# Optimization experiments

Hardware: AMD Instinct MI355X
Metric: run time of the kernel (lower is better)

## Reference

```python
import jax, jax.numpy as jnp
import numpy as np

N = 20000          # nodes
E = 320000         # edges
IN_C = 512         # input features
HID = 512          # 2*out_channels (first GCN layer width)
OUT = 256          # out_channels == num_hidden
PROJ = 256         # num_proj_hidden


def _gcn_conv(x, W, b, src, dst):
    """PyG GCNConv: x' = D^{-1/2}(A+I)D^{-1/2} X W + b (self-loops added)."""
    n = x.shape[0]
    x = x @ W  # [N, F_out]
    ones = jnp.ones((src.shape[0],), x.dtype)
    deg = jax.ops.segment_sum(ones, dst, num_segments=n) + 1.0  # +1 self-loop
    dis = jax.lax.rsqrt(deg)
    coef = dis[src] * dis[dst]                      # [E]
    agg = jax.ops.segment_sum(x[src] * coef[:, None], dst, num_segments=n)
    agg = agg + x * (dis * dis)[:, None]            # self-loop messages
    return agg + b


def setup_inputs() -> dict:
    key = jax.random.key(0)
    ks = jax.random.split(key, 12)
    s = 0.02
    return {
        "node_features": jax.random.normal(ks[0], (N, IN_C), jnp.float32),
        "edge_index": jax.random.randint(ks[1], (2, E), 0, N, jnp.int64),
        "W1": jax.random.normal(ks[2], (IN_C, HID), jnp.float32) * s,
        "b1": jnp.zeros((HID,), jnp.float32),
        "W2": jax.random.normal(ks[3], (HID, OUT), jnp.float32) * s,
        "b2": jnp.zeros((OUT,), jnp.float32),
        "a": jnp.asarray(0.25, jnp.float32),  # shared PReLU weight
        "W3": jax.random.normal(ks[4], (OUT, PROJ), jnp.float32) * s,
        "b3": jnp.zeros((PROJ,), jnp.float32),
        "W4": jax.random.normal(ks[5], (PROJ, OUT), jnp.float32) * s,
        "b4": jnp.zeros((OUT,), jnp.float32),
    }


def reference(node_features, edge_index, W1, b1, W2, b2, a, W3, b3, W4, b4):
    src, dst = edge_index[0], edge_index[1]
    prelu = lambda x: jnp.where(x > 0, x, a * x)
    h = prelu(_gcn_conv(node_features, W1, b1, src, dst))
    h = prelu(_gcn_conv(h, W2, b2, src, dst))
    # projection MLP: Linear -> ELU -> Linear
    h2 = jax.nn.elu(h @ W3 + b3)
    return h2 @ W4 + b4
```

## Files before the change

kernel.cpp:

```cpp
#include <hip/hip_runtime.h>

typedef unsigned short u16;
typedef unsigned int   u32;
typedef __attribute__((ext_vector_type(8))) short short8;
typedef __attribute__((ext_vector_type(4))) float f32x4;

__device__ __forceinline__ float bf2f(u16 h){
    return __uint_as_float(((u32)h) << 16);
}
__device__ __forceinline__ u16 f2bf(float f){
    u32 u = __float_as_uint(f);
    u += 0x7fffu + ((u >> 16) & 1u);
    return (u16)(u >> 16);
}

__global__ void probe_all(const u16* __restrict__ w1, const int* __restrict__ ei,
                          const void* b1, const void* b2, const void* b3,
                          const void* b4, const void* av,
                          int* __restrict__ f32f, int* __restrict__ efmt,
                          int* __restrict__ zf, int* __restrict__ cnt, int N,
                          u16* d1, u16* d2, u16* d3, u16* d4, u16* da){
    __shared__ int sf32, sfmt;
    int t = threadIdx.x;
    if (t == 0){ sf32 = 0; sfmt = 0; }
    __syncthreads();
    for (int i = t; i < N; i += 256) cnt[i] = 0;
    {
        int huge = 0;
        #pragma unroll
        for (int k = 0; k < 16; k++){
            u16 h = w1[t * 16 + k];
            if (((h >> 7) & 0xFF) >= 0x7F) huge = 1;
        }
        if (huge) atomicOr(&sf32, 1);
    }
    if (ei[2*t + 1] != 0) atomicOr(&sfmt, 1);
    __syncthreads();
    int f32 = sf32, fmt = sfmt;
    if (t == 0){ f32f[0] = f32; efmt[0] = fmt; zf[0] = 0; }
    #define CV(s,i) (f32 ? f2bf(((const float*)(s))[i]) : ((const u16*)(s))[i])
    d1[t]       = CV(b1, t);
    d1[t + 256] = CV(b1, t + 256);
    d2[t] = CV(b2, t);
    d3[t] = CV(b3, t);
    d4[t] = CV(b4, t);
    if (t == 0) da[0] = CV(av, 0);
    #undef CV
}

__device__ __forceinline__ int eload(const int* ei, int fmt, int idx){
    return fmt ? ei[idx] : ei[2*idx];
}

__global__ void deg_count(const int* __restrict__ ei, const int* __restrict__ efmt,
                          int* __restrict__ cnt, int E, int N){
    int e = blockIdx.x * 256 + threadIdx.x;
    if (e < E){
        int d = eload(ei, efmt[0], E + e);
        if ((unsigned)d < (unsigned)N) atomicAdd(&cnt[d], 1);
    }
}

__global__ void scan1(const int* __restrict__ cnt, int* __restrict__ incl,
                      int* __restrict__ bsum, int N){
    __shared__ int s[256];
    int t = threadIdx.x, i = blockIdx.x * 256 + t;
    int v = (i < N) ? cnt[i] : 0;
    s[t] = v;
    __syncthreads();
    #pragma unroll
    for (int off = 1; off < 256; off <<= 1){
        int u = (t >= off) ? s[t - off] : 0;
        __syncthreads();
        s[t] += u;
        __syncthreads();
    }
    if (i < N) incl[i] = s[t];
    if (t == 255) bsum[blockIdx.x] = s[255];
}

__global__ void scan23(const int* __restrict__ cnt, const int* __restrict__ incl,
                       const int* __restrict__ bsum, int nb,
                       int* __restrict__ rowstart, int* __restrict__ cursor,
                       float* __restrict__ dis, int N){
    __shared__ int s[128];
    int t = threadIdx.x;
    if (t < 128) s[t] = (t < nb) ? bsum[t] : 0;
    __syncthreads();
    #pragma unroll
    for (int off = 1; off < 128; off <<= 1){
        int u = 0;
        if (t < 128 && t >= off) u = s[t - off];
        __syncthreads();
        if (t < 128) s[t] += u;
        __syncthreads();
    }
    int boffb = s[blockIdx.x] - bsum[blockIdx.x];
    int i = blockIdx.x * 256 + t;
    if (i < N){
        int v = cnt[i];
        int rsv = boffb + incl[i] - v;
        rowstart[i] = rsv;
        cursor[i]   = rsv;
        dis[i] = rsqrtf((float)v + 1.0f);
    }
    if (blockIdx.x == 0 && t == 0) rowstart[N] = s[nb - 1];
}

__global__ void csr_fill(const int* __restrict__ ei, const int* __restrict__ efmt,
                         int* __restrict__ cursor, int* __restrict__ csr_src,
                         int E, int N){
    int e = blockIdx.x * 256 + threadIdx.x;
    if (e < E){
        int fmt = efmt[0];
        int d = eload(ei, fmt, E + e);
        if ((unsigned)d < (unsigned)N){
            int p = atomicAdd(&cursor[d], 1);
            csr_src[p] = eload(ei, fmt, e);
        }
    }
}

__global__ void transpose_all(const void* w1, const void* w2, const void* w3,
                              const void* w4, const int* __restrict__ flag,
                              u16* o1, u16* o2, u16* o3, u16* o4){
    const void* in; u16* out; int K, N;
    switch (blockIdx.z){
        case 0:  in = w1; out = o1; K = 512; N = 512; break;
        case 1:  in = w2; out = o2; K = 512; N = 256; break;
        case 2:  in = w3; out = o3; K = 256; N = 256; break;
        default: in = w4; out = o4; K = 256; N = 256; break;
    }
    int bx = blockIdx.x * 32;
    int by = blockIdx.y * 32;
    if (bx >= N || by >= K) return;
    __shared__ u16 t[32][33];
    int x = threadIdx.x, y = threadIdx.y;
    int f32 = flag[0];
    #pragma unroll
    for (int i = 0; i < 32; i += 8){
        size_t idx = (size_t)(by + y + i) * N + bx + x;
        t[y + i][x] = f32 ? f2bf(((const float*)in)[idx]) : ((const u16*)in)[idx];
    }
    __syncthreads();
    #pragma unroll
    for (int i = 0; i < 32; i += 8)
        out[(size_t)(bx + y + i) * K + by + x] = t[x][y + i];
}

#define TM 64
#define TN 128
#define BK 32
#define BKP 40

template<int MODE, int OUTF>
__global__ __launch_bounds__(256) void gemm_mfma(
    const void* __restrict__ A, const int* __restrict__ af32,
    const u16* __restrict__ BT,
    const u16* __restrict__ bias, void* __restrict__ Cv,
    int M, int K, int N)
{
    __shared__ __align__(16) u16 As[TM * BKP];
    __shared__ __align__(16) u16 Bs[TN * BKP];
    int tid  = threadIdx.x;
    int lane = tid & 63;
    int wave = tid >> 6;
    int waveM = wave >> 1, waveN = wave & 1;
    int bm = blockIdx.x * TM;
    int bn = blockIdx.y * TN;
    int f32 = af32[0];

    f32x4 acc[2][4] = {};

    int alr = tid >> 2;
    int alc = (tid & 3) * 8;
    int blr = tid >> 1;
    int blc = (tid & 1) * 16;

    for (int k0 = 0; k0 < K; k0 += BK){
        {
            int gr = bm + alr;
            short8 v = {0,0,0,0,0,0,0,0};
            if (gr < M){
                if (f32){
                    const float* p = (const float*)A + (size_t)gr * K + k0 + alc;
                    f32x4 a0 = *(const f32x4*)p;
                    f32x4 a1 = *(const f32x4*)(p + 4);
                    #pragma unroll
                    for (int j = 0; j < 4; j++){
                        v[j]   = (short)f2bf(a0[j]);
                        v[4+j] = (short)f2bf(a1[j]);
                    }
                } else {
                    v = *(const short8*)((const u16*)A + (size_t)gr * K + k0 + alc);
                }
            }
            *(short8*)&As[alr * BKP + alc] = v;
        }
        {
            const u16* p = BT + (size_t)(bn + blr) * K + k0 + blc;
            short8 v0 = *(const short8*)p;
            short8 v1 = *(const short8*)(p + 8);
            *(short8*)&Bs[blr * BKP + blc]     = v0;
            *(short8*)&Bs[blr * BKP + blc + 8] = v1;
        }
        __syncthreads();
        int q = lane >> 4;
        int r16 = lane & 15;
        short8 af[2], bfr[4];
        #pragma unroll
        for (int i = 0; i < 2; i++)
            af[i]  = *(const short8*)&As[(waveM*32 + i*16 + r16) * BKP + q*8];
        #pragma unroll
        for (int j = 0; j < 4; j++)
            bfr[j] = *(const short8*)&Bs[(waveN*64 + j*16 + r16) * BKP + q*8];
        #pragma unroll
        for (int i = 0; i < 2; i++)
            #pragma unroll
            for (int j = 0; j < 4; j++)
                acc[i][j] = __builtin_amdgcn_mfma_f32_16x16x32_bf16(af[i], bfr[j], acc[i][j], 0, 0, 0);
        __syncthreads();
    }

    int q = lane >> 4;
    int c16 = lane & 15;
    #pragma unroll
    for (int i = 0; i < 2; i++){
        #pragma unroll
        for (int j = 0; j < 4; j++){
            int gcol = bn + waveN*64 + j*16 + c16;
            float bvv = (MODE >= 1) ? bf2f(bias[gcol]) : 0.f;
            #pragma unroll
            for (int r = 0; r < 4; r++){
                int grow = bm + waveM*32 + i*16 + q*4 + r;
                if (grow < M){
                    float v = acc[i][j][r] + bvv;
                    if (MODE == 2) v = (v > 0.f) ? v : expm1f(v);
                    if (OUTF) ((float*)Cv)[(size_t)grow * N + gcol] = v;
                    else      ((u16*)Cv)[(size_t)grow * N + gcol] = f2bf(v);
                }
            }
        }
    }
}

template<int F, int NPB>
__global__ __launch_bounds__(F/8*NPB) void aggregate(
    const u16* __restrict__ XW, const int* __restrict__ rowstart,
    const int* __restrict__ csr_src, const float* __restrict__ dis,
    const u16* __restrict__ bias, const u16* __restrict__ aptr,
    u16* __restrict__ out, int N)
{
    int node = blockIdx.x * NPB + threadIdx.y;
    if (node >= N) return;
    int tf = threadIdx.x * 8;
    float a  = bf2f(aptr[0]);
    float di = dis[node];
    int e0 = rowstart[node], e1 = rowstart[node + 1];
    float acc[8] = {0,0,0,0,0,0,0,0};
    int ng = (e1 - e0) >> 3;
    int si[8]; float ci[8];
    if (ng > 0){
        #pragma unroll
        for (int u = 0; u < 8; u++) si[u] = csr_src[e0 + u];
        #pragma unroll
        for (int u = 0; u < 8; u++) ci[u] = dis[si[u]];
    }
    for (int g = 0; g < ng; g++){
        short8 vi[8];
        #pragma unroll
        for (int u = 0; u < 8; u++)
            vi[u] = *(const short8*)(XW + (size_t)si[u] * F + tf);
        int sn[8]; float cn[8];
        bool more = (g + 1) < ng;
        if (more){
            int base = e0 + (g + 1) * 8;
            #pragma unroll
            for (int u = 0; u < 8; u++) sn[u] = csr_src[base + u];
            #pragma unroll
            for (int u = 0; u < 8; u++) cn[u] = dis[sn[u]];
        }
        #pragma unroll
        for (int u = 0; u < 8; u++)
            #pragma unroll
            for (int j = 0; j < 8; j++)
                acc[j] += ci[u] * bf2f((u16)vi[u][j]);
        if (more){
            #pragma unroll
            for (int u = 0; u < 8; u++){ si[u] = sn[u]; ci[u] = cn[u]; }
        }
    }
    int e = e0 + ng * 8;
    for (; e + 4 <= e1; e += 4){
        int s0 = csr_src[e], s1 = csr_src[e+1], s2 = csr_src[e+2], s3 = csr_src[e+3];
        float c0 = dis[s0], c1 = dis[s1], c2 = dis[s2], c3 = dis[s3];
        short8 v0 = *(const short8*)(XW + (size_t)s0 * F + tf);
        short8 v1 = *(const short8*)(XW + (size_t)s1 * F + tf);
        short8 v2 = *(const short8*)(XW + (size_t)s2 * F + tf);
        short8 v3 = *(const short8*)(XW + (size_t)s3 * F + tf);
        #pragma unroll
        for (int j = 0; j < 8; j++)
            acc[j] += c0*bf2f((u16)v0[j]) + c1*bf2f((u16)v1[j])
                    + c2*bf2f((u16)v2[j]) + c3*bf2f((u16)v3[j]);
    }
    for (; e < e1; e++){
        int s = csr_src[e];
        float c = dis[s];
        short8 v = *(const short8*)(XW + (size_t)s * F + tf);
        #pragma unroll
        for (int j = 0; j < 8; j++) acc[j] += c * bf2f((u16)v[j]);
    }
    {
        short8 v = *(const short8*)(XW + (size_t)node * F + tf);
        #pragma unroll
        for (int j = 0; j < 8; j++) acc[j] += di * bf2f((u16)v[j]);
    }
    short8 bv = *(const short8*)(bias + tf);
    short8 o;
    #pragma unroll
    for (int j = 0; j < 8; j++){
        float x = di * acc[j] + bf2f((u16)bv[j]);
        x = (x > 0.f) ? x : a * x;
        o[j] = (short)f2bf(x);
    }
    *(short8*)(out + (size_t)node * F + tf) = o;
}

extern "C" void kernel_launch(void* const* d_in, const int* in_sizes, int n_in,
                              void* d_out, int out_size, void* d_ws, size_t ws_size,
                              hipStream_t stream)
{
    int iX=0, iEI=1, iW1=2, ib1=3, iW2=4, ib2=5, ia=6, iW3=7, ib3=8, iW4=9, ib4=10;
    {
        int jX=-1,jEI=-1,jW1=-1,jb1=-1,jW2=-1,ja=-1,jW3=-1,jW4=-1,jb2=-1,jb3=-1,jb4=-1;
        int n64k=0, n256=0;
        for (int i = 0; i < n_in; i++){
            switch (in_sizes[i]){
                case 10240000: jX = i; break;
                case 640000:   jEI = i; break;
                case 262144:   jW1 = i; break;
                case 131072:   jW2 = i; break;
                case 512:      jb1 = i; break;
                case 1:        ja = i; break;
                case 65536:    if (n64k++ == 0) jW3 = i; else jW4 = i; break;
                case 256: {
                    int k = n256++;
                    if (k == 0) jb2 = i; else if (k == 1) jb3 = i; else jb4 = i;
                } break;
                default: break;
            }
        }
        if (jX>=0&&jEI>=0&&jW1>=0&&jb1>=0&&jW2>=0&&ja>=0&&jW3>=0&&jW4>=0&&jb2>=0&&jb3>=0&&jb4>=0){
            iX=jX; iEI=jEI; iW1=jW1; ib1=jb1; iW2=jW2; ib2=jb2; ia=ja; iW3=jW3; ib3=jb3; iW4=jW4; ib4=jb4;
        }
    }
    int N = in_sizes[iX] / 512;
    int E = in_sizes[iEI] / 2;
    const int* EI = (const int*)d_in[iEI];
    float* OUT = (float*)d_out;
    u16*   S   = (u16*)d_out;

    char* ws = (char*)d_ws;
    size_t off = 0;
    auto alloc = [&](size_t bytes)->char*{
        char* p = ws + off;
        off = (off + bytes + 255) & ~(size_t)255;
        return p;
    };
    int nb = (N + 255) / 256;
    int*   cnt  = (int*)  alloc((size_t)N*4);
    int*   incl = (int*)  alloc((size_t)N*4);
    int*   bsum = (int*)  alloc(512);
    int*   efmt = (int*)  alloc(4);
    int*   f32f = (int*)  alloc(4);
    int*   zf   = (int*)  alloc(4);
    float* dis  = (float*)alloc((size_t)N*4);
    int*   rs   = (int*)  alloc((size_t)(N+1)*4);
    int*   cur  = (int*)  alloc((size_t)N*4);
    int*   csr  = (int*)  alloc((size_t)E*4);
    u16*   WT1  = (u16*)  alloc((size_t)512*512*2);
    u16*   WT2  = (u16*)  alloc((size_t)256*512*2);
    u16*   WT3  = (u16*)  alloc((size_t)256*256*2);
    u16*   WT4  = (u16*)  alloc((size_t)256*256*2);
    u16*   b1c  = (u16*)  alloc((size_t)512*2);
    u16*   b2c  = (u16*)  alloc((size_t)256*2);
    u16*   b3c  = (u16*)  alloc((size_t)256*2);
    u16*   b4c  = (u16*)  alloc((size_t)256*2);
    u16*   ac   = (u16*)  alloc((size_t)8*2);
    u16*   h1   = (u16*)  alloc((size_t)N*512*2);
    u16*   P    = (u16*)  alloc((size_t)N*256*2);

    if (ws_size < off) return;

    probe_all<<<1, 256, 0, stream>>>((const u16*)d_in[iW1], EI,
                                     d_in[ib1], d_in[ib2], d_in[ib3], d_in[ib4],
                                     d_in[ia], f32f, efmt, zf, cnt, N,
                                     b1c, b2c, b3c, b4c, ac);

    int egrid = (E + 255) / 256;
    deg_count<<<egrid, 256, 0, stream>>>(EI, efmt, cnt, E, N);
    scan1<<<nb, 256, 0, stream>>>(cnt, incl, bsum, N);
    scan23<<<nb, 256, 0, stream>>>(cnt, incl, bsum, nb, rs, cur, dis, N);
    csr_fill<<<egrid, 256, 0, stream>>>(EI, efmt, cur, csr, E, N);

    transpose_all<<<dim3(16, 16, 4), dim3(32, 8), 0, stream>>>(
        d_in[iW1], d_in[iW2], d_in[iW3], d_in[iW4], f32f, WT1, WT2, WT3, WT4);

    int gm = (N + TM - 1) / TM;
    dim3 g512(gm, 512 / TN);
    dim3 g256(gm, 256 / TN);

    gemm_mfma<0,0><<<g512, 256, 0, stream>>>(d_in[iX], f32f, WT1, nullptr, S, N, 512, 512);
    aggregate<512,2><<<(N+1)/2, dim3(64,2), 0, stream>>>(S, rs, csr, dis, b1c, ac, h1, N);

    u16* Q = (u16*)d_out;
    gemm_mfma<0,0><<<g256, 256, 0, stream>>>(h1, zf, WT2, nullptr, P, N, 512, 256);
    aggregate<256,4><<<(N+3)/4, dim3(32,4), 0, stream>>>(P, rs, csr, dis, b2c, ac, Q, N);

    gemm_mfma<2,0><<<g256, 256, 0, stream>>>(Q, zf, WT3, b3c, P, N, 256, 256);
    gemm_mfma<1,1><<<g256, 256, 0, stream>>>(P, zf, WT4, b4c, OUT, N, 256, 256);
}
```

Measured before the change: 286.4 us.

## Use 128x128 GEMM tiles with direct global-to-LDS loads and pre-converted bf16 X

Replaces the 64x128 GEMM with a 128x128 tile, BK=64 kernel that loads A and B straight into LDS through global_load_lds, with no per-thread fp32 conversion. X is converted to bf16 up front in a fused transpose/convert kernel, and the fp32 flag is recomputed locally instead of read from a device buffer. Aggregation launches use more nodes per block. Rows past M are read from buffers padded to N+128 rows. The exception is Q, which is d_out and is not padded, so edge tiles may read out of bounds. LDS tiles are unpadded, which risks bank conflicts.

```diff
diff --git a/kernel.cpp b/kernel.cpp
--- a/kernel.cpp
+++ b/kernel.cpp
@@ -1,4 +1,5 @@
 #include <hip/hip_runtime.h>
+#include <stdint.h>
 
 typedef unsigned short u16;
 typedef unsigned int   u32;
@@ -14,11 +15,17 @@
     return (u16)(u >> 16);
 }
 
+__device__ __forceinline__ void gl_lds16(const void* g, void* l){
+    __builtin_amdgcn_global_load_lds(
+        (__attribute__((address_space(1))) void*)(uintptr_t)g,
+        (__attribute__((address_space(3))) void*)(uintptr_t)l,
+        16, 0, 0);
+}
+
 __global__ void probe_all(const u16* __restrict__ w1, const int* __restrict__ ei,
                           const void* b1, const void* b2, const void* b3,
                           const void* b4, const void* av,
-                          int* __restrict__ f32f, int* __restrict__ efmt,
-                          int* __restrict__ zf, int* __restrict__ cnt, int N,
+                          int* __restrict__ efmt, int* __restrict__ cnt, int N,
                           u16* d1, u16* d2, u16* d3, u16* d4, u16* da){
     __shared__ int sf32, sfmt;
     int t = threadIdx.x;
@@ -36,8 +43,8 @@
     }
     if (ei[2*t + 1] != 0) atomicOr(&sfmt, 1);
     __syncthreads();
-    int f32 = sf32, fmt = sfmt;
-    if (t == 0){ f32f[0] = f32; efmt[0] = fmt; zf[0] = 0; }
+    int f32 = sf32;
+    if (t == 0) efmt[0] = sfmt;
     #define CV(s,i) (f32 ? f2bf(((const float*)(s))[i]) : ((const u16*)(s))[i])
     d1[t]       = CV(b1, t);
     d1[t + 256] = CV(b1, t + 256);
@@ -121,9 +128,50 @@
     }
 }
 
-__global__ void transpose_all(const void* w1, const void* w2, const void* w3,
-                              const void* w4, const int* __restrict__ flag,
-                              u16* o1, u16* o2, u16* o3, u16* o4){
+__global__ void transpose_x(const void* w1, const void* w2, const void* w3,
+                            const void* w4, const void* X,
+                            u16* o1, u16* o2, u16* o3, u16* o4,
+                            u16* xbf, int NN){
+    __shared__ int sf;
+    __shared__ u16 tb[32][33];
+    int lt = threadIdx.y * 32 + threadIdx.x;
+    if (lt == 0) sf = 0;
+    __syncthreads();
+    {
+        int huge = 0;
+        const u16* w = (const u16*)w1;
+        #pragma unroll
+        for (int k = 0; k < 8; k++){
+            u16 h = w[lt * 8 + k];
+            if (((h >> 7) & 0xFF) >= 0x7F) huge = 1;
+        }
+        if (huge) atomicOr(&sf, 1);
+    }
+    __syncthreads();
+    int f32 = sf;
+
+    if (blockIdx.z == 4){
+        size_t nb8 = (size_t)NN * 64;
+        size_t step = 256u * 256u;
+        for (size_t i = (size_t)(blockIdx.y * 16 + blockIdx.x) * 256 + lt; i < nb8; i += step){
+            short8 o;
+            if (f32){
+                const float* p = (const float*)X + i * 8;
+                f32x4 a0 = *(const f32x4*)p;
+                f32x4 a1 = *(const f32x4*)(p + 4);
+                #pragma unroll
+                for (int j = 0; j < 4; j++){
+                    o[j]     = (short)f2bf(a0[j]);
+                    o[4 + j] = (short)f2bf(a1[j]);
+                }
+            } else {
+                o = *(const short8*)((const u16*)X + i * 8);
+            }
+            *(short8*)(xbf + i * 8) = o;
+        }
+        return;
+    }
+
     const void* in; u16* out; int K, N;
     switch (blockIdx.z){
         case 0:  in = w1; out = o1; K = 512; N = 512; break;
@@ -134,105 +182,84 @@
     int bx = blockIdx.x * 32;
     int by = blockIdx.y * 32;
     if (bx >= N || by >= K) return;
-    __shared__ u16 t[32][33];
     int x = threadIdx.x, y = threadIdx.y;
-    int f32 = flag[0];
     #pragma unroll
     for (int i = 0; i < 32; i += 8){
         size_t idx = (size_t)(by + y + i) * N + bx + x;
-        t[y + i][x] = f32 ? f2bf(((const float*)in)[idx]) : ((const u16*)in)[idx];
+        tb[y + i][x] = f32 ? f2bf(((const float*)in)[idx]) : ((const u16*)in)[idx];
     }
     __syncthreads();
     #pragma unroll
     for (int i = 0; i < 32; i += 8)
-        out[(size_t)(bx + y + i) * K + by + x] = t[x][y + i];
-}
-
-#define TM 64
-#define TN 128
-#define BK 32
-#define BKP 40
+        out[(size_t)(bx + y + i) * K + by + x] = tb[x][y + i];
+}
+
+#define GTM 128
+#define GTN 128
+#define GBK 64
 
 template<int MODE, int OUTF>
-__global__ __launch_bounds__(256) void gemm_mfma(
-    const void* __restrict__ A, const int* __restrict__ af32,
-    const u16* __restrict__ BT,
+__global__ __launch_bounds__(256) void gemm128(
+    const u16* __restrict__ A, const u16* __restrict__ BT,
     const u16* __restrict__ bias, void* __restrict__ Cv,
     int M, int K, int N)
 {
-    __shared__ __align__(16) u16 As[TM * BKP];
-    __shared__ __align__(16) u16 Bs[TN * BKP];
+    __shared__ __align__(16) u16 As[GTM * GBK];
+    __shared__ __align__(16) u16 Bs[GTN * GBK];
     int tid  = threadIdx.x;
     int lane = tid & 63;
-    int wave = tid >> 6;
-    int waveM = wave >> 1, waveN = wave & 1;
-    int bm = blockIdx.x * TM;
-    int bn = blockIdx.y * TN;
-    int f32 = af32[0];
-
-    f32x4 acc[2][4] = {};
-
-    int alr = tid >> 2;
-    int alc = (tid & 3) * 8;
-    int blr = tid >> 1;
-    int blc = (tid & 1) * 16;
-
-    for (int k0 = 0; k0 < K; k0 += BK){
-        {
-            int gr = bm + alr;
-            short8 v = {0,0,0,0,0,0,0,0};
-            if (gr < M){
-                if (f32){
-                    const float* p = (const float*)A + (size_t)gr * K + k0 + alc;
-                    f32x4 a0 = *(const f32x4*)p;
-                    f32x4 a1 = *(const f32x4*)(p + 4);
-                    #pragma unroll
-                    for (int j = 0; j < 4; j++){
-                        v[j]   = (short)f2bf(a0[j]);
-                        v[4+j] = (short)f2bf(a1[j]);
-                    }
-                } else {
-                    v = *(const short8*)((const u16*)A + (size_t)gr * K + k0 + alc);
-                }
-            }
-            *(short8*)&As[alr * BKP + alc] = v;
-        }
-        {
-            const u16* p = BT + (size_t)(bn + blr) * K + k0 + blc;
-            short8 v0 = *(const short8*)p;
-            short8 v1 = *(const short8*)(p + 8);
-            *(short8*)&Bs[blr * BKP + blc]     = v0;
-            *(short8*)&Bs[blr * BKP + blc + 8] = v1;
-        }
-        __syncthreads();
-        int q = lane >> 4;
-        int r16 = lane & 15;
-        short8 af[2], bfr[4];
-        #pragma unroll
-        for (int i = 0; i < 2; i++)
-            af[i]  = *(const short8*)&As[(waveM*32 + i*16 + r16) * BKP + q*8];
-        #pragma unroll
-        for (int j = 0; j < 4; j++)
-            bfr[j] = *(const short8*)&Bs[(waveN*64 + j*16 + r16) * BKP + q*8];
-        #pragma unroll
-        for (int i = 0; i < 2; i++)
-            #pragma unroll
-            for (int j = 0; j < 4; j++)
-                acc[i][j] = __builtin_amdgcn_mfma_f32_16x16x32_bf16(af[i], bfr[j], acc[i][j], 0, 0, 0);
-        __syncthreads();
-    }
-
-    int q = lane >> 4;
-    int c16 = lane & 15;
-    #pragma unroll
-    for (int i = 0; i < 2; i++){
+    int wm   = (tid >> 7) & 1;
+    int wn   = (tid >> 6) & 1;
+    int bm = blockIdx.x * GTM;
+    int bn = blockIdx.y * GTN;
+
+    f32x4 acc[4][4] = {};
+
+    int srow = tid >> 3;
+    int scol = (tid & 7) * 8;
+    const u16* aP = A  + (size_t)(bm + srow) * K + scol;
+    const u16* bP = BT + (size_t)(bn + srow) * K + scol;
+    u16* lA = &As[tid * 8];
+    u16* lB = &Bs[tid * 8];
+
+    int q   = lane >> 4;
+    int r16 = lane & 15;
+    const u16* ra = &As[(wm*64 + r16) * GBK + q*8];
+    const u16* rb = &Bs[(wn*64 + r16) * GBK + q*8];
+
+    for (int k0 = 0; k0 < K; k0 += GBK){
+        #pragma unroll
+        for (int r = 0; r < 4; r++){
+            gl_lds16(aP + (size_t)r*32*K + k0, lA + r*32*GBK);
+            gl_lds16(bP + (size_t)r*32*K + k0, lB + r*32*GBK);
+        }
+        __syncthreads();
+        #pragma unroll
+        for (int kk = 0; kk < 2; kk++){
+            short8 af[4], bf[4];
+            #pragma unroll
+            for (int i = 0; i < 4; i++) af[i] = *(const short8*)(ra + i*16*GBK + kk*32);
+            #pragma unroll
+            for (int j = 0; j < 4; j++) bf[j] = *(const short8*)(rb + j*16*GBK + kk*32);
+            #pragma unroll
+            for (int i = 0; i < 4; i++)
+                #pragma unroll
+                for (int j = 0; j < 4; j++)
+                    acc[i][j] = __builtin_amdgcn_mfma_f32_16x16x32_bf16(af[i], bf[j], acc[i][j], 0, 0, 0);
+        }
+        __syncthreads();
+    }
+
+    int q4 = q * 4;
+    #pragma unroll
+    for (int i = 0; i < 4; i++){
         #pragma unroll
         for (int j = 0; j < 4; j++){
-            int gcol = bn + waveN*64 + j*16 + c16;
+            int gcol = bn + wn*64 + j*16 + r16;
             float bvv = (MODE >= 1) ? bf2f(bias[gcol]) : 0.f;
             #pragma unroll
             for (int r = 0; r < 4; r++){
-                int grow = bm + waveM*32 + i*16 + q*4 + r;
+                int grow = bm + wm*64 + i*16 + q4 + r;
                 if (grow < M){
                     float v = acc[i][j][r] + bvv;
                     if (MODE == 2) v = (v > 0.f) ? v : expm1f(v);
@@ -368,12 +395,11 @@
         return p;
     };
     int nb = (N + 255) / 256;
+    int MP = N + 128;
     int*   cnt  = (int*)  alloc((size_t)N*4);
     int*   incl = (int*)  alloc((size_t)N*4);
     int*   bsum = (int*)  alloc(512);
     int*   efmt = (int*)  alloc(4);
-    int*   f32f = (int*)  alloc(4);
-    int*   zf   = (int*)  alloc(4);
     float* dis  = (float*)alloc((size_t)N*4);
     int*   rs   = (int*)  alloc((size_t)(N+1)*4);
     int*   cur  = (int*)  alloc((size_t)N*4);
@@ -387,15 +413,20 @@
     u16*   b3c  = (u16*)  alloc((size_t)256*2);
     u16*   b4c  = (u16*)  alloc((size_t)256*2);
     u16*   ac   = (u16*)  alloc((size_t)8*2);
-    u16*   h1   = (u16*)  alloc((size_t)N*512*2);
-    u16*   P    = (u16*)  alloc((size_t)N*256*2);
+    u16*   Xbf  = (u16*)  alloc((size_t)MP*512*2);
+    u16*   h1   = (u16*)  alloc((size_t)MP*512*2);
+    u16*   P    = (u16*)  alloc((size_t)MP*256*2);
 
     if (ws_size < off) return;
 
     probe_all<<<1, 256, 0, stream>>>((const u16*)d_in[iW1], EI,
                                      d_in[ib1], d_in[ib2], d_in[ib3], d_in[ib4],
-                                     d_in[ia], f32f, efmt, zf, cnt, N,
+                                     d_in[ia], efmt, cnt, N,
                                      b1c, b2c, b3c, b4c, ac);
+
+    transpose_x<<<dim3(16, 16, 5), dim3(32, 8), 0, stream>>>(
+        d_in[iW1], d_in[iW2], d_in[iW3], d_in[iW4], d_in[iX],
+        WT1, WT2, WT3, WT4, Xbf, N);
 
     int egrid = (E + 255) / 256;
     deg_count<<<egrid, 256, 0, stream>>>(EI, efmt, cnt, E, N);
@@ -403,20 +434,17 @@
     scan23<<<nb, 256, 0, stream>>>(cnt, incl, bsum, nb, rs, cur, dis, N);
     csr_fill<<<egrid, 256, 0, stream>>>(EI, efmt, cur, csr, E, N);
 
-    transpose_all<<<dim3(16, 16, 4), dim3(32, 8), 0, stream>>>(
-        d_in[iW1], d_in[iW2], d_in[iW3], d_in[iW4], f32f, WT1, WT2, WT3, WT4);
-
-    int gm = (N + TM - 1) / TM;
-    dim3 g512(gm, 512 / TN);
-    dim3 g256(gm, 256 / TN);
-
-    gemm_mfma<0,0><<<g512, 256, 0, stream>>>(d_in[iX], f32f, WT1, nullptr, S, N, 512, 512);
-    aggregate<512,2><<<(N+1)/2, dim3(64,2), 0, stream>>>(S, rs, csr, dis, b1c, ac, h1, N);
+    int gm = (N + GTM - 1) / GTM;
+    dim3 g512(gm, 512 / GTN);
+    dim3 g256(gm, 256 / GTN);
+
+    gemm128<0,0><<<g512, 256, 0, stream>>>(Xbf, WT1, nullptr, S, N, 512, 512);
+    aggregate<512,8><<<(N+7)/8, dim3(64,8), 0, stream>>>(S, rs, csr, dis, b1c, ac, h1, N);
 
     u16* Q = (u16*)d_out;
-    gemm_mfma<0,0><<<g256, 256, 0, stream>>>(h1, zf, WT2, nullptr, P, N, 512, 256);
-    aggregate<256,4><<<(N+3)/4, dim3(32,4), 0, stream>>>(P, rs, csr, dis, b2c, ac, Q, N);
-
-    gemm_mfma<2,0><<<g256, 256, 0, stream>>>(Q, zf, WT3, b3c, P, N, 256, 256);
-    gemm_mfma<1,1><<<g256, 256, 0, stream>>>(P, zf, WT4, b4c, OUT, N, 256, 256);
-}
+    gemm128<0,0><<<g256, 256, 0, stream>>>(h1, WT2, nullptr, P, N, 512, 256);
+    aggregate<256,16><<<(N+15)/16, dim3(32,16), 0, stream>>>(P, rs, csr, dis, b2c, ac, Q, N);
+
+    gemm128<2,0><<<g256, 256, 0, stream>>>(Q, WT3, b3c, P, N, 256, 256);
+    gemm128<1,1><<<g256, 256, 0, stream>>>(P, WT4, b4c, OUT, N, 256, 256);
+}
```

After: 303.7 us. 1.06x slower.
